# Kernel optimization log

Measured on AMD Instinct MI355X. Metric: run time of the kernel, lower is better.

The kernel has to match this reference:

```python
import jax, jax.numpy as jnp
import numpy as np

B, N, F = 4, 1024, 512        # batch, tokens, features
H, D = 8, 64                  # heads, attention_dim (= value dim here)
E = 16                        # edge feature dim
LN_EPS = 1e-5


def setup_inputs() -> dict:
    key = jax.random.key(0)
    ks = jax.random.split(key, 9)
    receiver_input = jax.random.normal(ks[0], (B, N, F), dtype=jnp.float32)
    edge_features = jax.random.normal(ks[1], (B, N, N, E), dtype=jnp.float32)
    mask = (jax.random.uniform(ks[2], (B, N, N)) > 0.5).astype(jnp.float32)
    s = 1.0 / np.sqrt(F)
    Wq = jax.random.normal(ks[3], (F, H * D), dtype=jnp.float32) * s
    Wk = jax.random.normal(ks[4], (F, H * D), dtype=jnp.float32) * s
    Wv = jax.random.normal(ks[5], (F, H * D), dtype=jnp.float32) * s
    We = jax.random.normal(ks[6], (E, H), dtype=jnp.float32) * (1.0 / np.sqrt(E))
    Wo = jax.random.normal(ks[7], (H * D, H * D), dtype=jnp.float32) * (1.0 / np.sqrt(H * D))
    ln_scale = jnp.ones((F,), dtype=jnp.float32)
    ln_offset = jnp.zeros((F,), dtype=jnp.float32)
    return {
        "receiver_input": receiver_input, "edge_features": edge_features,
        "mask": mask, "ln_scale": ln_scale, "ln_offset": ln_offset,
        "Wq": Wq, "Wk": Wk, "Wv": Wv, "We": We, "Wo": Wo,
    }


def _layer_norm(x, scale, offset):
    mu = jnp.mean(x, axis=-1, keepdims=True)
    var = jnp.var(x, axis=-1, keepdims=True)
    return (x - mu) * jax.lax.rsqrt(var + LN_EPS) * scale + offset


def reference(receiver_input, edge_features, mask, ln_scale, ln_offset, Wq, Wk, Wv, We, Wo):
    r = _layer_norm(receiver_input, ln_scale, ln_offset)   # sender = receiver (self-attn)
    q = (r @ Wq).reshape(B, N, H, D)
    k = (r @ Wk).reshape(B, N, H, D)
    v = (r @ Wv).reshape(B, N, H, D)
    # logits [b, i, j, h]; edge bias added BEFORE softmax (over senders j = axis -2)
    logits = jnp.einsum("bihf,bjhf->bijh", q, k) + edge_features @ We
    w = jax.nn.softmax(logits, axis=-2)
    w = w * mask[..., None]                                 # post-softmax mask multiply
    out = jnp.einsum("bijh,bjhv->bihv", w, v)
    out = out.reshape(B, N, H * D) * (1.0 / jnp.sqrt(jnp.float32(D)))
    out = out @ Wo
    out = out + receiver_input                              # residual (shapes match: F == H*D)
    return out
```

## Files before the change

kernel.cpp:

```cpp
#include <hip/hip_runtime.h>

#define BB 4
#define NN 1024
#define FF 512
#define HH 8
#define DD 64
#define EE 16

typedef unsigned short u16;
typedef _Float16 f16;
typedef __attribute__((ext_vector_type(8))) _Float16 f16x8;
typedef __attribute__((ext_vector_type(4))) float     f32x4;

#define MFMAH(a,b,c) __builtin_amdgcn_mfma_f32_16x16x32_f16((a),(b),(c),0,0,0)

static __device__ __forceinline__ void gld16(const void* g, void* l){
  __builtin_amdgcn_global_load_lds((const __attribute__((address_space(1))) unsigned int*)g,
                                   (__attribute__((address_space(3))) unsigned int*)l, 16, 0, 0);
}

__global__ __launch_bounds__(256) void k_wsplit(
    const float* __restrict__ Wq, const float* __restrict__ Wk,
    const float* __restrict__ Wv, const float* __restrict__ Wo,
    f16* __restrict__ WT, f16* __restrict__ WoT){
  __shared__ float tile[32][33];
  int bid = blockIdx.x, t = threadIdx.x;
  int isA = bid < 768;
  int tb  = isA ? bid : bid - 768;
  int nct = isA ? 48 : 16;
  int ct = tb % nct, ft = tb / nct;
  int c0 = ct * 32, f0 = ft * 32;
  #pragma unroll
  for (int r4 = 0; r4 < 4; r4++){
    int fl = (t >> 5) * 4 + r4, cl = t & 31;
    int f = f0 + fl, c = c0 + cl;
    float v;
    if (isA){
      const float* W = (c < 512) ? Wq : ((c < 1024) ? Wk : Wv);
      v = W[f * 512 + (c & 511)];
    } else {
      v = Wo[f * 512 + c];
    }
    tile[fl][cl] = v;
  }
  __syncthreads();
  #pragma unroll
  for (int r4 = 0; r4 < 4; r4++){
    int cl = (t >> 5) * 4 + r4, fl = t & 31;
    float v = tile[fl][cl];
    int c = c0 + cl, f = f0 + fl;
    if (isA) WT[c * 512 + f]  = (f16)v;
    else     WoT[c * 512 + f] = (f16)v;
  }
}

__global__ __launch_bounds__(256) void k_ln(
    const float* __restrict__ x, const float* __restrict__ gamma,
    const float* __restrict__ beta, f16* __restrict__ rf){
  int row  = blockIdx.x * 4 + (threadIdx.x >> 6);
  int lane = threadIdx.x & 63;
  const float* px = x + (size_t)row * 512 + lane * 8;
  float4 a = *(const float4*)px;
  float4 b = *(const float4*)(px + 4);
  float v[8] = {a.x,a.y,a.z,a.w,b.x,b.y,b.z,b.w};
  float s = 0.f, q = 0.f;
  #pragma unroll
  for (int j = 0; j < 8; j++){ s += v[j]; q += v[j]*v[j]; }
  #pragma unroll
  for (int m = 1; m < 64; m <<= 1){ s += __shfl_xor(s, m, 64); q += __shfl_xor(q, m, 64); }
  float mean = s * (1.f/512.f);
  float var  = q * (1.f/512.f) - mean * mean;
  float rstd = rsqrtf(var + 1e-5f);
  float4 ga = *(const float4*)(gamma + lane*8);
  float4 gb = *(const float4*)(gamma + lane*8 + 4);
  float4 b0 = *(const float4*)(beta  + lane*8);
  float4 b1 = *(const float4*)(beta  + lane*8 + 4);
  float gs[8] = {ga.x,ga.y,ga.z,ga.w,gb.x,gb.y,gb.z,gb.w};
  float bs[8] = {b0.x,b0.y,b0.z,b0.w,b1.x,b1.y,b1.z,b1.w};
  f16x8 hv;
  #pragma unroll
  for (int j = 0; j < 8; j++){
    float r = (v[j] - mean) * rstd * gs[j] + bs[j];
    hv[j] = (f16)r;
  }
  *(f16x8*)(rf + (size_t)row * 512 + lane * 8) = hv;
}

__global__ __launch_bounds__(256) void k_qkv(
    const f16* __restrict__ rf, const f16* __restrict__ WT,
    f16* __restrict__ qf, f16* __restrict__ kf, f16* __restrict__ vT){
  __shared__ f16 As[128*32], Bs[128*32];
  int bid = blockIdx.x;
  int mt = bid & 31, nt = bid >> 5;
  int m0 = mt << 7,  n0 = nt << 7;
  int t = threadIdx.x, lane = t & 63, w = t >> 6;
  int wm = (w >> 1) << 6, wn = (w & 1) << 6;
  int fr = lane & 15, g = lane >> 4;
  f32x4 acc[4][4];
  #pragma unroll
  for (int i = 0; i < 4; i++)
    #pragma unroll
    for (int j = 0; j < 4; j++) acc[i][j] = (f32x4){0.f,0.f,0.f,0.f};

  for (int k0 = 0; k0 < 512; k0 += 32){
    #pragma unroll
    for (int q = 0; q < 2; q++){
      int c = ((q << 2) + w) * 64 + lane;
      int row = c >> 2, part = c & 3;
      int ldso = ((q << 2) + w) * 512;
      gld16(rf + (size_t)(m0+row)*512 + k0 + part*8, &As[ldso]);
      gld16(WT + (size_t)(n0+row)*512 + k0 + part*8, &Bs[ldso]);
    }
    __syncthreads();
    f16x8 a[4], b[4];
    #pragma unroll
    for (int mi = 0; mi < 4; mi++) a[mi] = *(const f16x8*)&As[(wm + mi*16 + fr)*32 + g*8];
    #pragma unroll
    for (int ni = 0; ni < 4; ni++) b[ni] = *(const f16x8*)&Bs[(wn + ni*16 + fr)*32 + g*8];
    #pragma unroll
    for (int mi = 0; mi < 4; mi++)
      #pragma unroll
      for (int ni = 0; ni < 4; ni++)
        acc[mi][ni] = MFMAH(a[mi], b[ni], acc[mi][ni]);
    __syncthreads();
  }
  #pragma unroll
  for (int mi = 0; mi < 4; mi++)
    #pragma unroll
    for (int ni = 0; ni < 4; ni++)
      #pragma unroll
      for (int r = 0; r < 4; r++){
        int gm = m0 + wm + mi*16 + g*4 + r;
        int gc = n0 + wn + ni*16 + fr;
        float vv = acc[mi][ni][r];
        int b = gm >> 10, i = gm & 1023;
        int mat = gc >> 9, h = (gc >> 6) & 7, d = gc & 63;
        size_t idx = ((size_t)((b << 3) + h) * 1024 + i) * 64 + d;
        if      (mat == 0) qf[idx] = (f16)vv;
        else if (mat == 1) kf[idx] = (f16)vv;
        else vT[((size_t)((b << 3) + h) * 64 + d) * 1024 + i] = (f16)vv;
      }
}

__global__ __launch_bounds__(512) void k_attn(
    const float* __restrict__ edge, const float* __restrict__ mask,
    const float* __restrict__ We,
    const f16* __restrict__ qf, const f16* __restrict__ kf,
    const f16* __restrict__ vT, f16* __restrict__ part_o,
    float2* __restrict__ part_md){
  __shared__ float We_s[128];
  __shared__ float bias_s[2][8][16*33];
  __shared__ float mask_s[2][16*33];
  __shared__ f16   pm_s[8][16*40];

  int bid = blockIdx.x;
  int s  = bid & 3;
  int i0 = ((bid >> 2) & 63) << 4;
  int b  = bid >> 8;
  int t = threadIdx.x, lane = t & 63, w = t >> 6;
  int fr = lane & 15, g = lane >> 4;
  if (t < 128) We_s[t] = We[t];

  size_t qb = ((size_t)((b << 3) + w) * 1024 + i0 + fr) * 64 + g * 8;
  f16x8 qf0 = *(const f16x8*)(qf + qb);
  f16x8 qf1 = *(const f16x8*)(qf + qb + 32);

  f32x4 oacc[4];
  #pragma unroll
  for (int vf = 0; vf < 4; vf++) oacc[vf] = (f32x4){0.f,0.f,0.f,0.f};
  float mrun[4], den[4];
  #pragma unroll
  for (int r = 0; r < 4; r++){ mrun[r] = -3e38f; den[r] = 0.f; }

  int pi = t >> 5, pj = t & 31;
  const float* ebase = edge + ((size_t)(b*1024 + i0 + pi) * 1024 + s*256 + pj) * 16;
  const float* mbase = mask + (size_t)(b*1024 + i0 + pi) * 1024 + s*256 + pj;

  float4 e0 = *(const float4*)(ebase);
  float4 e1 = *(const float4*)(ebase + 4);
  float4 e2 = *(const float4*)(ebase + 8);
  float4 e3 = *(const float4*)(ebase + 12);
  float  mval = *mbase;
  __syncthreads();
  {
    float ef[16] = {e0.x,e0.y,e0.z,e0.w, e1.x,e1.y,e1.z,e1.w,
                    e2.x,e2.y,e2.z,e2.w, e3.x,e3.y,e3.z,e3.w};
    float bias[8] = {0.f,0.f,0.f,0.f,0.f,0.f,0.f,0.f};
    #pragma unroll
    for (int e = 0; e < 16; e++){
      float ev = ef[e];
      #pragma unroll
      for (int h = 0; h < 8; h++) bias[h] += ev * We_s[e*8 + h];
    }
    #pragma unroll
    for (int h = 0; h < 8; h++) bias_s[0][h][pi*33 + pj] = bias[h];
    mask_s[0][pi*33 + pj] = mval;
  }
  __syncthreads();
  int cur = 0;

  #pragma unroll 1
  for (int jt = 0; jt < 8; jt++){
    int j0 = s*256 + (jt << 5);

    size_t kb0 = ((size_t)((b << 3) + w) * 1024 + j0 + fr) * 64 + g * 8;
    size_t kb1 = kb0 + 16 * 64;
    f16x8 kf00 = *(const f16x8*)(kf + kb0);
    f16x8 kf01 = *(const f16x8*)(kf + kb0 + 32);
    f16x8 kf10 = *(const f16x8*)(kf + kb1);
    f16x8 kf11 = *(const f16x8*)(kf + kb1 + 32);
    f16x8 vfr[4];
    #pragma unroll
    for (int vf = 0; vf < 4; vf++)
      vfr[vf] = *(const f16x8*)(vT + ((size_t)((b << 3) + w) * 64 + vf*16 + fr) * 1024 + j0 + g*8);
    __builtin_amdgcn_sched_barrier(0);

    if (jt < 7){
      const float* ep = ebase + (size_t)((jt + 1) << 5) * 16;
      e0 = *(const float4*)(ep);
      e1 = *(const float4*)(ep + 4);
      e2 = *(const float4*)(ep + 8);
      e3 = *(const float4*)(ep + 12);
      mval = mbase[(jt + 1) << 5];
    }
    __builtin_amdgcn_sched_barrier(0);

    float bs0[4], bs1[4], ms0[4], ms1[4];
    #pragma unroll
    for (int r = 0; r < 4; r++){
      int row = g*4 + r;
      bs0[r] = bias_s[cur][w][row*33 + fr];
      bs1[r] = bias_s[cur][w][row*33 + 16 + fr];
      ms0[r] = mask_s[cur][row*33 + fr];
      ms1[r] = mask_s[cur][row*33 + 16 + fr];
    }

    f32x4 lg0 = (f32x4){0.f,0.f,0.f,0.f};
    f32x4 lg1 = (f32x4){0.f,0.f,0.f,0.f};
    lg0 = MFMAH(qf0, kf00, lg0); lg1 = MFMAH(qf0, kf10, lg1);
    lg0 = MFMAH(qf1, kf01, lg0); lg1 = MFMAH(qf1, kf11, lg1);

    float tm[4];
    #pragma unroll
    for (int r = 0; r < 4; r++){
      lg0[r] += bs0[r];
      lg1[r] += bs1[r];
      tm[r] = fmaxf(lg0[r], lg1[r]);
    }
    #pragma unroll
    for (int mk = 1; mk < 16; mk <<= 1){
      #pragma unroll
      for (int r = 0; r < 4; r++) tm[r] = fmaxf(tm[r], __shfl_xor(tm[r], mk, 16));
    }
    float p0[4], p1[4], scl[4], ps[4];
    #pragma unroll
    for (int r = 0; r < 4; r++){
      float nm = fmaxf(mrun[r], tm[r]);
      scl[r] = exp2f((mrun[r] - nm) * 1.44269504089f);
      mrun[r] = nm;
      p0[r] = exp2f((lg0[r] - nm) * 1.44269504089f);
      p1[r] = exp2f((lg1[r] - nm) * 1.44269504089f);
      ps[r] = p0[r] + p1[r];
    }
    #pragma unroll
    for (int mk = 1; mk < 16; mk <<= 1){
      #pragma unroll
      for (int r = 0; r < 4; r++) ps[r] += __shfl_xor(ps[r], mk, 16);
    }
    #pragma unroll
    for (int r = 0; r < 4; r++) den[r] = den[r] * scl[r] + ps[r];
    #pragma unroll
    for (int vf = 0; vf < 4; vf++)
      #pragma unroll
      for (int r = 0; r < 4; r++) oacc[vf][r] *= scl[r];

    #pragma unroll
    for (int r = 0; r < 4; r++){
      int row = g*4 + r;
      pm_s[w][row*40 + fr]      = (f16)(p0[r] * ms0[r]);
      pm_s[w][row*40 + 16 + fr] = (f16)(p1[r] * ms1[r]);
    }
    asm volatile("s_waitcnt lgkmcnt(0)" ::: "memory");
    f16x8 pa = *(const f16x8*)&pm_s[w][fr*40 + g*8];
    #pragma unroll
    for (int vf = 0; vf < 4; vf++)
      oacc[vf] = MFMAH(pa, vfr[vf], oacc[vf]);

    if (jt < 7){
      float ef[16] = {e0.x,e0.y,e0.z,e0.w, e1.x,e1.y,e1.z,e1.w,
                      e2.x,e2.y,e2.z,e2.w, e3.x,e3.y,e3.z,e3.w};
      float bias[8] = {0.f,0.f,0.f,0.f,0.f,0.f,0.f,0.f};
      #pragma unroll
      for (int e = 0; e < 16; e++){
        float ev = ef[e];
        #pragma unroll
        for (int h = 0; h < 8; h++) bias[h] += ev * We_s[e*8 + h];
      }
      int nxt = cur ^ 1;
      #pragma unroll
      for (int h = 0; h < 8; h++) bias_s[nxt][h][pi*33 + pj] = bias[h];
      mask_s[nxt][pi*33 + pj] = mval;
    }
    __syncthreads();
    cur ^= 1;
  }

  float id[4];
  #pragma unroll
  for (int r = 0; r < 4; r++) id[r] = 1.0f / den[r];
  int bh = (b << 3) + w;
  #pragma unroll
  for (int vf = 0; vf < 4; vf++)
    #pragma unroll
    for (int r = 0; r < 4; r++){
      int row = g*4 + r;
      part_o[((size_t)((s*32 + bh) * 1024) + i0 + row) * 64 + vf*16 + fr] =
          (f16)(oacc[vf][r] * id[r]);
    }
  if (fr == 0){
    #pragma unroll
    for (int r = 0; r < 4; r++){
      int row = g*4 + r;
      part_md[(size_t)(s*32 + bh) * 1024 + i0 + row] = make_float2(mrun[r], den[r]);
    }
  }
}

__global__ __launch_bounds__(256) void k_combine(
    const f16* __restrict__ part_o, const float2* __restrict__ part_md,
    f16* __restrict__ AO){
  int wg   = blockIdx.x * 4 + (threadIdx.x >> 6);
  int lane = threadIdx.x & 63;
  int bh = wg >> 10, i = wg & 1023;
  int b = bh >> 3, h = bh & 7;
  float2 md[4];
  float M = -3e38f;
  #pragma unroll
  for (int s = 0; s < 4; s++){
    md[s] = part_md[(size_t)(s*32 + bh) * 1024 + i];
    M = fmaxf(M, md[s].x);
  }
  float wsum = 0.f, o = 0.f;
  #pragma unroll
  for (int s = 0; s < 4; s++){
    float wq = md[s].y * exp2f((md[s].x - M) * 1.44269504089f);
    wsum += wq;
    o += wq * (float)part_o[((size_t)((s*32 + bh) * 1024) + i) * 64 + lane];
  }
  AO[((size_t)(b*1024 + i)) * 512 + h*64 + lane] = (f16)(o * 0.125f / wsum);
}

__global__ __launch_bounds__(256) void k_out(
    const f16* __restrict__ AO, const f16* __restrict__ WoT,
    const float* __restrict__ x, float* __restrict__ out){
  __shared__ f16 As[64*32], Bs[128*32];
  int bid = blockIdx.x;
  int mt = bid & 63, nt = bid >> 6;
  int m0 = mt << 6, n0 = nt << 7;
  int t = threadIdx.x, lane = t & 63, w = t >> 6;
  int wm = (w >> 1) << 5, wn = (w & 1) << 6;
  int fr = lane & 15, g = lane >> 4;
  f32x4 acc[2][4];
  #pragma unroll
  for (int i = 0; i < 2; i++)
    #pragma unroll
    for (int j = 0; j < 4; j++) acc[i][j] = (f32x4){0.f,0.f,0.f,0.f};

  for (int k0 = 0; k0 < 512; k0 += 32){
    {
      int row = t >> 2, part = t & 3;
      gld16(AO + (size_t)(m0+row)*512 + k0 + part*8, &As[w*512]);
    }
    #pragma unroll
    for (int q = 0; q < 2; q++){
      int c = ((q << 2) + w) * 64 + lane;
      int row = c >> 2, part = c & 3;
      gld16(WoT + (size_t)(n0+row)*512 + k0 + part*8, &Bs[((q<<2)+w)*512]);
    }
    __syncthreads();
    f16x8 af[2], bf_[4];
    #pragma unroll
    for (int mi = 0; mi < 2; mi++) af[mi]  = *(const f16x8*)&As[(wm + mi*16 + fr)*32 + g*8];
    #pragma unroll
    for (int ni = 0; ni < 4; ni++) bf_[ni] = *(const f16x8*)&Bs[(wn + ni*16 + fr)*32 + g*8];
    #pragma unroll
    for (int mi = 0; mi < 2; mi++)
      #pragma unroll
      for (int ni = 0; ni < 4; ni++)
        acc[mi][ni] = MFMAH(af[mi], bf_[ni], acc[mi][ni]);
    __syncthreads();
  }
  #pragma unroll
  for (int mi = 0; mi < 2; mi++)
    #pragma unroll
    for (int ni = 0; ni < 4; ni++)
      #pragma unroll
      for (int r = 0; r < 4; r++){
        size_t gm = m0 + wm + mi*16 + g*4 + r;
        size_t gn = n0 + wn + ni*16 + fr;
        out[gm*512 + gn] = acc[mi][ni][r] + x[gm*512 + gn];
      }
}

extern "C" void kernel_launch(void* const* d_in, const int* in_sizes, int n_in,
                              void* d_out, int out_size, void* d_ws, size_t ws_size,
                              hipStream_t stream){
  const float* xin   = (const float*)d_in[0];
  const float* edge  = (const float*)d_in[1];
  const float* mask  = (const float*)d_in[2];
  const float* gamma = (const float*)d_in[3];
  const float* beta  = (const float*)d_in[4];
  const float* Wq    = (const float*)d_in[5];
  const float* Wk    = (const float*)d_in[6];
  const float* Wv    = (const float*)d_in[7];
  const float* We    = (const float*)d_in[8];
  const float* Wo    = (const float*)d_in[9];
  float* out = (float*)d_out;

  f16* p   = (f16*)d_ws;
  f16* WT  = p;                 p += 1536*512;
  f16* WoT = p;                 p += 512*512;
  f16* rf  = p;                 p += 4096*512;
  f16* qf  = p;                 p += 2097152;
  f16* kf  = p;                 p += 2097152;
  f16* vT  = p;                 p += 2097152;
  f16* AO  = p;                 p += 2097152;
  f16* part_o = p;              p += 8388608;
  float2* part_md = (float2*)p;

  k_wsplit <<<1024, 256, 0, stream>>>(Wq, Wk, Wv, Wo, WT, WoT);
  k_ln     <<<1024, 256, 0, stream>>>(xin, gamma, beta, rf);
  k_qkv    <<<384,  256, 0, stream>>>(rf, WT, qf, kf, vT);
  k_attn   <<<1024, 512, 0, stream>>>(edge, mask, We, qf, kf, vT, part_o, part_md);
  k_combine<<<8192, 256, 0, stream>>>(part_o, part_md, AO);
  k_out    <<<256,  256, 0, stream>>>(AO, WoT, xin, out);
}
```

Measured before the change: 193.9 us.

## Precompute edge bias into swizzled fp16 buffer and drop split-KV combine

Moves the edge-feature projection and mask conversion into a separate kernel that writes fp16 bias and mask in the exact per-lane MFMA fragment order. The attention kernel then loads these directly with no shared-memory staging or barriers, processes all 1024 keys per wave instead of splitting across four blocks, and writes the final normalized output, which removes the combine kernel and its partial buffers. In exchange it writes and rereads a 64MB bias buffer, launches only 512 blocks of 4 independent waves for attention, and rounds the bias to fp16.

```diff
diff --git a/kernel.cpp b/kernel.cpp
--- a/kernel.cpp
+++ b/kernel.cpp
@@ -142,29 +142,79 @@
       }
 }
 
-__global__ __launch_bounds__(512) void k_attn(
+__global__ __launch_bounds__(256) void k_bias(
     const float* __restrict__ edge, const float* __restrict__ mask,
     const float* __restrict__ We,
+    f16* __restrict__ bias_sw, f16* __restrict__ mask_sw){
+  __shared__ float We_s[128];
+  int t = threadIdx.x;
+  if (t < 128) We_s[t] = We[t];
+  __syncthreads();
+  int bid = blockIdx.x;
+  int jtp = bid & 15, it = (bid >> 4) & 63, b = bid >> 10;
+  int lane = t & 63, sub = t >> 6;
+  int jt = jtp * 2 + (sub & 1);
+  int hq = sub >> 1;
+  int fr = lane & 15, g = lane >> 4;
+
+  float acc[4][8];
+  float mv[8];
+  #pragma unroll
+  for (int p = 0; p < 8; p++){
+    int r = p & 3, colh = p >> 2;
+    int i = it*16 + g*4 + r;
+    int j = jt*32 + fr + colh*16;
+    const float* ep = edge + ((size_t)(b*1024 + i) * 1024 + j) * 16;
+    float4 e0 = *(const float4*)(ep);
+    float4 e1 = *(const float4*)(ep + 4);
+    float4 e2 = *(const float4*)(ep + 8);
+    float4 e3 = *(const float4*)(ep + 12);
+    float ef[16] = {e0.x,e0.y,e0.z,e0.w, e1.x,e1.y,e1.z,e1.w,
+                    e2.x,e2.y,e2.z,e2.w, e3.x,e3.y,e3.z,e3.w};
+    if (hq == 0) mv[p] = mask[(size_t)(b*1024 + i) * 1024 + j];
+    #pragma unroll
+    for (int hh = 0; hh < 4; hh++){
+      float a = 0.f;
+      #pragma unroll
+      for (int e = 0; e < 16; e++) a += ef[e] * We_s[e*8 + hq*4 + hh];
+      acc[hh][p] = a;
+    }
+  }
+  #pragma unroll
+  for (int hh = 0; hh < 4; hh++){
+    f16x8 o;
+    #pragma unroll
+    for (int p = 0; p < 8; p++) o[p] = (f16)acc[hh][p];
+    *(f16x8*)(bias_sw + (((size_t)(b*8 + hq*4 + hh) * 64 + it) * 32 + jt) * 512 + lane*8) = o;
+  }
+  if (hq == 0){
+    f16x8 o;
+    #pragma unroll
+    for (int p = 0; p < 8; p++) o[p] = (f16)mv[p];
+    *(f16x8*)(mask_sw + (((size_t)(b*64 + it)) * 32 + jt) * 512 + lane*8) = o;
+  }
+}
+
+__global__ __launch_bounds__(256) void k_attn(
+    const f16* __restrict__ bias_sw, const f16* __restrict__ mask_sw,
     const f16* __restrict__ qf, const f16* __restrict__ kf,
-    const f16* __restrict__ vT, f16* __restrict__ part_o,
-    float2* __restrict__ part_md){
-  __shared__ float We_s[128];
-  __shared__ float bias_s[2][8][16*33];
-  __shared__ float mask_s[2][16*33];
-  __shared__ f16   pm_s[8][16*40];
-
-  int bid = blockIdx.x;
-  int s  = bid & 3;
-  int i0 = ((bid >> 2) & 63) << 4;
-  int b  = bid >> 8;
+    const f16* __restrict__ vT, f16* __restrict__ AO){
+  __shared__ f16 pm_s[4][16*40];
   int t = threadIdx.x, lane = t & 63, w = t >> 6;
+  int wid = blockIdx.x * 4 + w;
+  int b = wid >> 9, h = (wid >> 6) & 7, it = wid & 63;
   int fr = lane & 15, g = lane >> 4;
-  if (t < 128) We_s[t] = We[t];
-
-  size_t qb = ((size_t)((b << 3) + w) * 1024 + i0 + fr) * 64 + g * 8;
+  int bh = b*8 + h;
+
+  size_t qb = ((size_t)bh * 1024 + it*16 + fr) * 64 + g*8;
   f16x8 qf0 = *(const f16x8*)(qf + qb);
   f16x8 qf1 = *(const f16x8*)(qf + qb + 32);
 
+  const f16* bbase = bias_sw + ((size_t)bh * 2048 + it*32) * 512 + lane*8;
+  const f16* mbase = mask_sw + ((size_t)(b*64 + it) * 32) * 512 + lane*8;
+  const f16* kbase = kf + (size_t)bh * 65536;
+  const f16* vbase = vT + (size_t)bh * 65536;
+
   f32x4 oacc[4];
   #pragma unroll
   for (int vf = 0; vf < 4; vf++) oacc[vf] = (f32x4){0.f,0.f,0.f,0.f};
@@ -172,68 +222,20 @@
   #pragma unroll
   for (int r = 0; r < 4; r++){ mrun[r] = -3e38f; den[r] = 0.f; }
 
-  int pi = t >> 5, pj = t & 31;
-  const float* ebase = edge + ((size_t)(b*1024 + i0 + pi) * 1024 + s*256 + pj) * 16;
-  const float* mbase = mask + (size_t)(b*1024 + i0 + pi) * 1024 + s*256 + pj;
-
-  float4 e0 = *(const float4*)(ebase);
-  float4 e1 = *(const float4*)(ebase + 4);
-  float4 e2 = *(const float4*)(ebase + 8);
-  float4 e3 = *(const float4*)(ebase + 12);
-  float  mval = *mbase;
-  __syncthreads();
-  {
-    float ef[16] = {e0.x,e0.y,e0.z,e0.w, e1.x,e1.y,e1.z,e1.w,
-                    e2.x,e2.y,e2.z,e2.w, e3.x,e3.y,e3.z,e3.w};
-    float bias[8] = {0.f,0.f,0.f,0.f,0.f,0.f,0.f,0.f};
-    #pragma unroll
-    for (int e = 0; e < 16; e++){
-      float ev = ef[e];
-      #pragma unroll
-      for (int h = 0; h < 8; h++) bias[h] += ev * We_s[e*8 + h];
-    }
-    #pragma unroll
-    for (int h = 0; h < 8; h++) bias_s[0][h][pi*33 + pj] = bias[h];
-    mask_s[0][pi*33 + pj] = mval;
-  }
-  __syncthreads();
-  int cur = 0;
-
   #pragma unroll 1
-  for (int jt = 0; jt < 8; jt++){
-    int j0 = s*256 + (jt << 5);
-
-    size_t kb0 = ((size_t)((b << 3) + w) * 1024 + j0 + fr) * 64 + g * 8;
-    size_t kb1 = kb0 + 16 * 64;
-    f16x8 kf00 = *(const f16x8*)(kf + kb0);
-    f16x8 kf01 = *(const f16x8*)(kf + kb0 + 32);
-    f16x8 kf10 = *(const f16x8*)(kf + kb1);
-    f16x8 kf11 = *(const f16x8*)(kf + kb1 + 32);
+  for (int jt = 0; jt < 32; jt++){
+    int j0 = jt << 5;
+    f16x8 bias16 = *(const f16x8*)(bbase + jt*512);
+    f16x8 msk16  = *(const f16x8*)(mbase + jt*512);
+    const f16* kp = kbase + (size_t)(j0 + fr) * 64 + g*8;
+    f16x8 kf00 = *(const f16x8*)(kp);
+    f16x8 kf01 = *(const f16x8*)(kp + 32);
+    f16x8 kf10 = *(const f16x8*)(kp + 16*64);
+    f16x8 kf11 = *(const f16x8*)(kp + 16*64 + 32);
     f16x8 vfr[4];
     #pragma unroll
     for (int vf = 0; vf < 4; vf++)
-      vfr[vf] = *(const f16x8*)(vT + ((size_t)((b << 3) + w) * 64 + vf*16 + fr) * 1024 + j0 + g*8);
-    __builtin_amdgcn_sched_barrier(0);
-
-    if (jt < 7){
-      const float* ep = ebase + (size_t)((jt + 1) << 5) * 16;
-      e0 = *(const float4*)(ep);
-      e1 = *(const float4*)(ep + 4);
-      e2 = *(const float4*)(ep + 8);
-      e3 = *(const float4*)(ep + 12);
-      mval = mbase[(jt + 1) << 5];
-    }
-    __builtin_amdgcn_sched_barrier(0);
-
-    float bs0[4], bs1[4], ms0[4], ms1[4];
-    #pragma unroll
-    for (int r = 0; r < 4; r++){
-      int row = g*4 + r;
-      bs0[r] = bias_s[cur][w][row*33 + fr];
-      bs1[r] = bias_s[cur][w][row*33 + 16 + fr];
-      ms0[r] = mask_s[cur][row*33 + fr];
-      ms1[r] = mask_s[cur][row*33 + 16 + fr];
-    }
+      vfr[vf] = *(const f16x8*)(vbase + (size_t)(vf*16 + fr) * 1024 + j0 + g*8);
 
     f32x4 lg0 = (f32x4){0.f,0.f,0.f,0.f};
     f32x4 lg1 = (f32x4){0.f,0.f,0.f,0.f};
@@ -243,8 +245,8 @@
     float tm[4];
     #pragma unroll
     for (int r = 0; r < 4; r++){
-      lg0[r] += bs0[r];
-      lg1[r] += bs1[r];
+      lg0[r] += (float)bias16[r];
+      lg1[r] += (float)bias16[4 + r];
       tm[r] = fmaxf(lg0[r], lg1[r]);
     }
     #pragma unroll
@@ -277,77 +279,26 @@
     #pragma unroll
     for (int r = 0; r < 4; r++){
       int row = g*4 + r;
-      pm_s[w][row*40 + fr]      = (f16)(p0[r] * ms0[r]);
-      pm_s[w][row*40 + 16 + fr] = (f16)(p1[r] * ms1[r]);
+      pm_s[w][row*40 + fr]      = (f16)(p0[r] * (float)msk16[r]);
+      pm_s[w][row*40 + 16 + fr] = (f16)(p1[r] * (float)msk16[4 + r]);
     }
     asm volatile("s_waitcnt lgkmcnt(0)" ::: "memory");
     f16x8 pa = *(const f16x8*)&pm_s[w][fr*40 + g*8];
     #pragma unroll
     for (int vf = 0; vf < 4; vf++)
       oacc[vf] = MFMAH(pa, vfr[vf], oacc[vf]);
-
-    if (jt < 7){
-      float ef[16] = {e0.x,e0.y,e0.z,e0.w, e1.x,e1.y,e1.z,e1.w,
-                      e2.x,e2.y,e2.z,e2.w, e3.x,e3.y,e3.z,e3.w};
-      float bias[8] = {0.f,0.f,0.f,0.f,0.f,0.f,0.f,0.f};
-      #pragma unroll
-      for (int e = 0; e < 16; e++){
-        float ev = ef[e];
-        #pragma unroll
-        for (int h = 0; h < 8; h++) bias[h] += ev * We_s[e*8 + h];
-      }
-      int nxt = cur ^ 1;
-      #pragma unroll
-      for (int h = 0; h < 8; h++) bias_s[nxt][h][pi*33 + pj] = bias[h];
-      mask_s[nxt][pi*33 + pj] = mval;
-    }
-    __syncthreads();
-    cur ^= 1;
   }
 
   float id[4];
   #pragma unroll
-  for (int r = 0; r < 4; r++) id[r] = 1.0f / den[r];
-  int bh = (b << 3) + w;
+  for (int r = 0; r < 4; r++) id[r] = 0.125f / den[r];
   #pragma unroll
   for (int vf = 0; vf < 4; vf++)
     #pragma unroll
     for (int r = 0; r < 4; r++){
-      int row = g*4 + r;
-      part_o[((size_t)((s*32 + bh) * 1024) + i0 + row) * 64 + vf*16 + fr] =
-          (f16)(oacc[vf][r] * id[r]);
-    }
-  if (fr == 0){
-    #pragma unroll
-    for (int r = 0; r < 4; r++){
-      int row = g*4 + r;
-      part_md[(size_t)(s*32 + bh) * 1024 + i0 + row] = make_float2(mrun[r], den[r]);
-    }
-  }
-}
-
-__global__ __launch_bounds__(256) void k_combine(
-    const f16* __restrict__ part_o, const float2* __restrict__ part_md,
-    f16* __restrict__ AO){
-  int wg   = blockIdx.x * 4 + (threadIdx.x >> 6);
-  int lane = threadIdx.x & 63;
-  int bh = wg >> 10, i = wg & 1023;
-  int b = bh >> 3, h = bh & 7;
-  float2 md[4];
-  float M = -3e38f;
-  #pragma unroll
-  for (int s = 0; s < 4; s++){
-    md[s] = part_md[(size_t)(s*32 + bh) * 1024 + i];
-    M = fmaxf(M, md[s].x);
-  }
-  float wsum = 0.f, o = 0.f;
-  #pragma unroll
-  for (int s = 0; s < 4; s++){
-    float wq = md[s].y * exp2f((md[s].x - M) * 1.44269504089f);
-    wsum += wq;
-    o += wq * (float)part_o[((size_t)((s*32 + bh) * 1024) + i) * 64 + lane];
-  }
-  AO[((size_t)(b*1024 + i)) * 512 + h*64 + lane] = (f16)(o * 0.125f / wsum);
+      int row = g*4 + r, d = vf*16 + fr;
+      AO[((size_t)(b*1024 + it*16 + row)) * 512 + h*64 + d] = (f16)(oacc[vf][r] * id[r]);
+    }
 }
 
 __global__ __launch_bounds__(256) void k_out(
@@ -418,20 +369,20 @@
   float* out = (float*)d_out;
 
   f16* p   = (f16*)d_ws;
-  f16* WT  = p;                 p += 1536*512;
-  f16* WoT = p;                 p += 512*512;
-  f16* rf  = p;                 p += 4096*512;
-  f16* qf  = p;                 p += 2097152;
-  f16* kf  = p;                 p += 2097152;
-  f16* vT  = p;                 p += 2097152;
-  f16* AO  = p;                 p += 2097152;
-  f16* part_o = p;              p += 8388608;
-  float2* part_md = (float2*)p;
-
-  k_wsplit <<<1024, 256, 0, stream>>>(Wq, Wk, Wv, Wo, WT, WoT);
-  k_ln     <<<1024, 256, 0, stream>>>(xin, gamma, beta, rf);
-  k_qkv    <<<384,  256, 0, stream>>>(rf, WT, qf, kf, vT);
-  k_attn   <<<1024, 512, 0, stream>>>(edge, mask, We, qf, kf, vT, part_o, part_md);
-  k_combine<<<8192, 256, 0, stream>>>(part_o, part_md, AO);
-  k_out    <<<256,  256, 0, stream>>>(AO, WoT, xin, out);
-}
+  f16* WT      = p;   p += 1536*512;
+  f16* WoT     = p;   p += 512*512;
+  f16* rf      = p;   p += 4096*512;
+  f16* qf      = p;   p += 2097152;
+  f16* kf      = p;   p += 2097152;
+  f16* vT      = p;   p += 2097152;
+  f16* bias_sw = p;   p += 33554432;
+  f16* mask_sw = p;   p += 4194304;
+  f16* AO      = rf;
+
+  k_wsplit<<<1024, 256, 0, stream>>>(Wq, Wk, Wv, Wo, WT, WoT);
+  k_ln    <<<1024, 256, 0, stream>>>(xin, gamma, beta, rf);
+  k_qkv   <<<384,  256, 0, stream>>>(rf, WT, qf, kf, vT);
+  k_bias  <<<4096, 256, 0, stream>>>(edge, mask, We, bias_sw, mask_sw);
+  k_attn  <<<512,  256, 0, stream>>>(bias_sw, mask_sw, qf, kf, vT, AO);
+  k_out   <<<256,  256, 0, stream>>>(AO, WoT, xin, out);
+}
```

New measurement: 275.8 us. 1.42x slower.
